# Performance work log

Measured on AMD Instinct MI355X. Metric: run time of the kernel, lower is better.

The kernel has to match this reference:

```python
import jax, jax.numpy as jnp
import numpy as np

G = 16                 # grid side -> 4096 voxels
N_GRID = G ** 3
N_NODES = 4096         # protein nodes
DEG = 256              # node neighbors per grid voxel
HID = 64               # MPNN hidden == ResNet in_channels
NUM_CLASSES = 20
BN = np.float32(1.0 / np.sqrt(1.0 + 1e-5))  # eval-mode BatchNorm3d (mean=0, var=1, gamma=1, beta=0)


def _lin(key, fi, fo):
    return jax.random.normal(key, (fi, fo), jnp.float32) * (fi ** -0.5)


def _cw(key, o, i, k):
    return jax.random.normal(key, (o, i, k, k, k), jnp.float32) * ((i * k ** 3) ** -0.5)


def setup_inputs() -> dict:
    key = jax.random.key(0)
    ks = jax.random.split(key, 32)
    n_edges = N_GRID * DEG
    # every grid voxel receives exactly DEG messages (bincount never zero)
    edge_i = jax.random.randint(ks[0], (n_edges,), 0, N_NODES, dtype=jnp.int32)
    edge_j = jnp.repeat(jnp.arange(N_GRID, dtype=jnp.int32), DEG)
    edge_index = jnp.stack([edge_i, edge_j])  # [2, E]

    node_embedding = jax.random.normal(ks[1], (N_NODES, HID), jnp.float32)
    node_pos = jax.random.uniform(ks[2], (N_NODES, 3), jnp.float32)
    gx = (jnp.arange(G, dtype=jnp.float32) + 0.5) / G
    gd, gh, gw = jnp.meshgrid(gx, gx, gx, indexing='ij')
    grid_pos = jnp.stack([gd, gh, gw], -1).reshape(N_GRID, 3)

    z = lambda n: jnp.zeros((n,), jnp.float32)
    return {
        'node_embedding': node_embedding, 'node_pos': node_pos,
        'grid_pos': grid_pos, 'edge_index': edge_index,
        # MPNN edge / message / update MLPs
        'ew1': _lin(ks[3], 6, HID), 'eb1': z(HID), 'ew2': _lin(ks[4], HID, HID), 'eb2': z(HID),
        'mw1': _lin(ks[5], 2 * HID, HID), 'mb1': z(HID), 'mw2': _lin(ks[6], HID, HID), 'mb2': z(HID),
        'uw1': _lin(ks[7], HID, HID), 'ub1': z(HID), 'uw2': _lin(ks[8], HID, HID), 'ub2': z(HID),
        # ResNet3D: 3 Blocks (conv3 a, conv3 b, conv5 shortcut) with channels 64->64, 64->128, 128->256
        'c1a': _cw(ks[9], 64, 64, 3), 'c1b': _cw(ks[10], 64, 64, 3), 'c1s': _cw(ks[11], 64, 64, 5),
        'c2a': _cw(ks[12], 128, 64, 3), 'c2b': _cw(ks[13], 128, 128, 3), 'c2s': _cw(ks[14], 128, 64, 5),
        'c3a': _cw(ks[15], 256, 128, 3), 'c3b': _cw(ks[16], 256, 256, 3), 'c3s': _cw(ks[17], 256, 128, 5),
        'fcw': _lin(ks[18], 256, NUM_CLASSES), 'fcb': z(NUM_CLASSES),
    }


def _mlp(x, w1, b1, w2, b2):
    return jax.nn.silu(x @ w1 + b1) @ w2 + b2


def _conv(x, w, p):
    return jax.lax.conv_general_dilated(
        x, w, window_strides=(1, 1, 1), padding=[(p, p)] * 3,
        dimension_numbers=('NCDHW', 'OIDHW', 'NCDHW'))


def _block(x, wa, wb, ws):
    out = jax.nn.relu(_conv(x, wa, 1) * BN)
    out = _conv(out, wb, 1) * BN
    sc = _conv(x, ws, 2) * BN
    return jax.nn.relu(out + sc)


def reference(node_embedding, node_pos, grid_pos, edge_index,
              ew1, eb1, ew2, eb2, mw1, mb1, mw2, mb2, uw1, ub1, uw2, ub2,
              c1a, c1b, c1s, c2a, c2b, c2s, c3a, c3b, c3s, fcw, fcb):
    i, j = edge_index[0], edge_index[1]
    # ---- MPNN: gather, edge MLP, message MLP, scatter-mean, update MLP ----
    edge_attr = jnp.concatenate([node_pos[i], grid_pos[j]], axis=-1)        # [E, 6]
    pos_emb = _mlp(edge_attr, ew1, eb1, ew2, eb2)                           # [E, H]
    msg = _mlp(jnp.concatenate([node_embedding[i], pos_emb], -1),
               mw1, mb1, mw2, mb2)                                          # [E, H]
    agg = jax.ops.segment_sum(msg, j, num_segments=N_GRID)                  # [N_GRID, H]
    cnt = jax.ops.segment_sum(jnp.ones((msg.shape[0],), msg.dtype), j,
                              num_segments=N_GRID)
    grid_feat = _mlp(agg / cnt[:, None], uw1, ub1, uw2, ub2)                # [N_GRID, H]
    # ---- ResNet3D over the grid volume ----
    x = grid_feat.T.reshape(1, HID, G, G, G) * BN                           # instance_norm1 (eval BN)
    x = _block(x, c1a, c1b, c1s)
    x = _block(x, c2a, c2b, c2s)
    x = _block(x, c3a, c3b, c3s)
    pooled = jnp.max(x, axis=(2, 3, 4))                                     # max_pool3d(kernel=spatial)
    return pooled @ fcw + fcb                                               # [1, NUM_CLASSES]
```

## Files before the change

### kernel.cpp

```cpp
#include <hip/hip_runtime.h>
#include <math.h>

#define BN_S 0.9999950000374997f

typedef _Float16 half8 __attribute__((ext_vector_type(8)));
typedef float f32x4 __attribute__((ext_vector_type(4)));

__device__ __forceinline__ float silu_f(float x) {
    return __fdividef(x, 1.0f + __expf(-x));
}

__device__ __forceinline__ void gld16(const void* g, void* l) {
    __builtin_amdgcn_global_load_lds(
        (const __attribute__((address_space(1))) void*)g,
        (__attribute__((address_space(3))) void*)l, 16, 0, 0);
}

__global__ __launch_bounds__(64) void prep_w_k(
    const float* __restrict__ ew2, const float* __restrict__ mw1,
    const float* __restrict__ mw2, const float* __restrict__ uw1,
    const float* __restrict__ mb2, const float* __restrict__ ub1,
    float* __restrict__ W_mu, float* __restrict__ b_mu,
    _Float16* __restrict__ wemt_h, _Float16* __restrict__ wemt_l)
{
    const int k = blockIdx.x, c = threadIdx.x;
    float s = 0.f;
    for (int m = 0; m < 64; m++) s = fmaf(ew2[k*64 + m], mw1[(64 + m)*64 + c], s);
    {
        const int q = k >> 5, kg = (k >> 3) & 3, jj = k & 7;
        const int sl = q*256 + c*4 + kg;
        const int p = sl ^ ((sl >> 3) & 7);
        const _Float16 h = (_Float16)s;
        const _Float16 l = (_Float16)(s - (float)h);
        wemt_h[p*8 + jj] = h;
        wemt_l[p*8 + jj] = l;
    }
    float s2 = 0.f;
    for (int m = 0; m < 64; m++) s2 = fmaf(mw2[k*64 + m], uw1[m*64 + c], s2);
    W_mu[k*64 + c] = s2;
    if (k == 0) {
        float s3 = ub1[c];
        for (int m = 0; m < 64; m++) s3 = fmaf(mb2[m], uw1[m*64 + c], s3);
        b_mu[c] = s3;
    }
}

__global__ __launch_bounds__(64) void prep_nodes_k(
    const float* __restrict__ node_embedding, const float* __restrict__ node_pos,
    const float* __restrict__ grid_pos, const float* __restrict__ ew1,
    const float* __restrict__ eb1, const float* __restrict__ mw1,
    const float* __restrict__ mb1, const float* __restrict__ eb2,
    float* __restrict__ a_node, float* __restrict__ g_vox, float* __restrict__ n_node)
{
    const int v = blockIdx.x, c = threadIdx.x;
    const float p0 = node_pos[v*3], p1 = node_pos[v*3 + 1], p2 = node_pos[v*3 + 2];
    a_node[v*64 + c] = fmaf(p0, ew1[c], fmaf(p1, ew1[64 + c], fmaf(p2, ew1[128 + c], eb1[c])));
    const float q0 = grid_pos[v*3], q1 = grid_pos[v*3 + 1], q2 = grid_pos[v*3 + 2];
    g_vox[v*64 + c] = fmaf(q0, ew1[192 + c], fmaf(q1, ew1[256 + c], q2 * ew1[320 + c]));
    float s = mb1[c];
    for (int k = 0; k < 64; k++) s = fmaf(node_embedding[v*64 + k], mw1[k*64 + c], s);
    for (int k = 0; k < 64; k++) s = fmaf(eb2[k], mw1[(64 + k)*64 + c], s);
    n_node[v*64 + c] = s;
}

template<int K3, int NCOG, int NCH>
__global__ __launch_bounds__(256) void wsplit_k(
    const float* __restrict__ w, _Float16* __restrict__ dh, _Float16* __restrict__ dl,
    int CI)
{
    __shared__ float s[32*K3];
    const int co = blockIdx.x, cig = blockIdx.y, t = threadIdx.x;
    const float* src = w + ((size_t)co*CI + cig*32)*K3;
    for (int m = t; m < 32*K3; m += 256) s[m] = src[m];
    __syncthreads();
    const int coG = co >> 6, col = co & 63;
    for (int m = t; m < 32*K3; m += 256) {
        const int tap = m >> 5, cil = m & 31;
        const float x = s[cil*K3 + tap];
        const _Float16 h = (_Float16)x;
        const _Float16 l = (_Float16)(x - (float)h);
        const int b = cil >> 3, jj = cil & 7;
        const int sl = col*4 + b;
        const int p = sl ^ ((sl >> 3) & 7);
        const size_t base = ((size_t)(tap*NCOG + coG)*NCH + cig) * 2048;
        dh[base + p*8 + jj] = h;
        dl[base + p*8 + jj] = l;
    }
}

__global__ __launch_bounds__(256) void edge_kernel(
    const int* __restrict__ edge_i,
    const float* __restrict__ a_node, const float* __restrict__ g_vox,
    const float* __restrict__ n_node,
    const _Float16* __restrict__ wemt_h, const _Float16* __restrict__ wemt_l,
    const float* __restrict__ W_mu, const float* __restrict__ b_mu,
    const float* __restrict__ uw2, const float* __restrict__ ub2,
    _Float16* __restrict__ x0h, _Float16* __restrict__ x0l)
{
    __shared__ __align__(16) _Float16 sAh[4096], sAl[4096];
    __shared__ __align__(16) _Float16 sBh[4096], sBl[4096];
    __shared__ float sV1[64], sV2[64];

    const int j = blockIdx.x, t = threadIdx.x;
    const int lane = t & 63, wv = t >> 6, ln15 = lane & 15, kg = lane >> 4;
    const int ebase = j << 8;

    gld16(wemt_h + t*8, &sAh[t*8]);
    gld16(wemt_h + 2048 + t*8, &sAh[2048 + t*8]);
    gld16(wemt_l + t*8, &sAl[t*8]);
    gld16(wemt_l + 2048 + t*8, &sAl[2048 + t*8]);

    const int r = t >> 2, sub = t & 3;
    float gv[16];
    #pragma unroll
    for (int m = 0; m < 16; m++) gv[m] = g_vox[j*64 + sub*16 + m];

    asm volatile("s_waitcnt vmcnt(0)" ::: "memory");
    __syncthreads();

    float psum[4] = {0.f, 0.f, 0.f, 0.f};

    for (int T = 0; T < 4; T++) {
        {
            const int i = edge_i[ebase + T*64 + r];
            float s1[16];
            #pragma unroll
            for (int m = 0; m < 16; m++)
                s1[m] = silu_f(a_node[i*64 + sub*16 + m] + gv[m]);
            half8 h0, l0, h1, l1;
            #pragma unroll
            for (int m = 0; m < 8; m++) {
                h0[m] = (_Float16)s1[m];
                l0[m] = (_Float16)(s1[m] - (float)h0[m]);
                h1[m] = (_Float16)s1[8 + m];
                l1[m] = (_Float16)(s1[8 + m] - (float)h1[m]);
            }
            const int q = sub >> 1, kg0 = (sub & 1) * 2;
            const int slot0 = (q*4 + kg0)*64 + r;
            *(half8*)&sBh[slot0*8] = h0; *(half8*)&sBl[slot0*8] = l0;
            *(half8*)&sBh[(slot0 + 64)*8] = h1; *(half8*)&sBl[(slot0 + 64)*8] = l1;
        }
        __syncthreads();
        #pragma unroll
        for (int eF = 0; eF < 4; eF++) {
            const int e = eF*16 + ln15;
            const int ie = edge_i[ebase + T*64 + e];
            f32x4 acc;
            {
                const float4 nv = *(const float4*)&n_node[(size_t)ie*64 + wv*16 + kg*4];
                acc[0] = nv.x; acc[1] = nv.y; acc[2] = nv.z; acc[3] = nv.w;
            }
            #pragma unroll
            for (int q = 0; q < 2; q++) {
                const int sa = q*256 + (wv*16 + ln15)*4 + kg;
                const int pa = sa ^ ((sa >> 3) & 7);
                const half8 Ah = *(const half8*)&sAh[pa*8];
                const half8 Al = *(const half8*)&sAl[pa*8];
                const int sb = ((q*4 + kg)*64 + e)*8;
                const half8 Bh = *(const half8*)&sBh[sb];
                const half8 Bl = *(const half8*)&sBl[sb];
                acc = __builtin_amdgcn_mfma_f32_16x16x32_f16(Ah, Bh, acc, 0, 0, 0);
                acc = __builtin_amdgcn_mfma_f32_16x16x32_f16(Ah, Bl, acc, 0, 0, 0);
                acc = __builtin_amdgcn_mfma_f32_16x16x32_f16(Al, Bh, acc, 0, 0, 0);
            }
            #pragma unroll
            for (int rg = 0; rg < 4; rg++) psum[rg] += silu_f(acc[rg]);
        }
        __syncthreads();
    }

    #pragma unroll
    for (int rg = 0; rg < 4; rg++) {
        float v = psum[rg];
        v += __shfl_xor(v, 1, 64); v += __shfl_xor(v, 2, 64);
        v += __shfl_xor(v, 4, 64); v += __shfl_xor(v, 8, 64);
        psum[rg] = v;
    }
    if (ln15 == 0) {
        #pragma unroll
        for (int rg = 0; rg < 4; rg++)
            sV1[wv*16 + kg*4 + rg] = psum[rg] * (1.0f / 256.0f);
    }
    __syncthreads();
    if (t < 64) {
        float h = b_mu[t];
        for (int k = 0; k < 64; k++) h = fmaf(sV1[k], W_mu[k*64 + t], h);
        sV2[t] = silu_f(h);
    }
    __syncthreads();
    if (t < 64) {
        float g = ub2[t];
        for (int k = 0; k < 64; k++) g = fmaf(sV2[k], uw2[k*64 + t], g);
        const float val = g * BN_S;
        const _Float16 hh = (_Float16)val;
        const _Float16 ll = (_Float16)(val - (float)hh);
        const int c = t, zz = j >> 8, v = j & 255;
        const size_t a16 = ((size_t)((c >> 5)*16 + zz)*1024 + ((c >> 3) & 3)*256 + v)*8 + (c & 7);
        x0h[a16] = hh; x0l[a16] = ll;
    }
}

template<int KK, int CI, int NCOG, int CIS>
__global__ __launch_bounds__(256) void conv_mfma_k(
    const _Float16* __restrict__ xh, const _Float16* __restrict__ xl,
    const _Float16* __restrict__ wh, const _Float16* __restrict__ wl,
    float* __restrict__ slab)
{
    constexpr int P = KK/2, K2 = KK*KK, NCH = CI/32, NCHS = NCH/CIS, CO = NCOG*64;
    const int d0 = blockIdx.x, coG = blockIdx.y;
    const int cis = blockIdx.z / KK, kd = blockIdx.z % KK;
    const int t = threadIdx.x;
    const int lane = t & 63, wv = t >> 6;
    const int ln15 = lane & 15, kg = lane >> 4;

    float* sout = slab + ((size_t)blockIdx.z*CO + coG*64)*4096 + d0*256;
    const int z = d0 + kd - P;
    if ((unsigned)z >= 16u) {
        for (int m = t; m < 64*256; m += 256)
            sout[(size_t)(m >> 8)*4096 + (m & 255)] = 0.f;
        return;
    }

    __shared__ __align__(16) _Float16 sXh[8192];
    __shared__ __align__(16) _Float16 sXl[8192];
    __shared__ __align__(16) _Float16 sAh[2][2048];
    __shared__ __align__(16) _Float16 sAl[2][2048];
    __shared__ __align__(16) _Float16 zb[8];
    if (t < 8) zb[t] = (_Float16)0.f;

    auto stage_X = [&](int ch) {
        const size_t b16 = ((size_t)ch*16 + z) * 8192;
        #pragma unroll
        for (int q = 0; q < 4; q++) {
            gld16(xh + b16 + (q*256 + t)*8, &sXh[(q*256 + t)*8]);
            gld16(xl + b16 + (q*256 + t)*8, &sXl[(q*256 + t)*8]);
        }
    };
    auto stage_A = [&](int ab, int ch, int t2) {
        const size_t b16 = ((size_t)((kd*K2 + t2)*NCOG + coG)*NCH + ch) * 2048;
        gld16(wh + b16 + t*8, &sAh[ab][t*8]);
        gld16(wl + b16 + t*8, &sAl[ab][t*8]);
    };

    f32x4 acc[4][4];
    #pragma unroll
    for (int a = 0; a < 4; a++)
        #pragma unroll
        for (int b = 0; b < 4; b++)
            #pragma unroll
            for (int r2 = 0; r2 < 4; r2++) acc[a][b][r2] = 0.f;

    const int ch0 = cis * NCHS;
    stage_A(0, ch0, 0);
    stage_X(ch0);
    asm volatile("s_waitcnt vmcnt(0)" ::: "memory");
    __syncthreads();

    int ap = 0;
    for (int cc = 0; cc < NCHS; cc++) {
        const int ch = ch0 + cc;
        for (int t2 = 0; t2 < K2; t2++) {
            if (t2 + 1 < K2) stage_A(ap ^ 1, ch, t2 + 1);
            else if (cc + 1 < NCHS) stage_A(ap ^ 1, ch + 1, 0);

            const int kh = t2 / KK, kw = t2 % KK;
            half8 Afh[4], Afl[4];
            #pragma unroll
            for (int cf = 0; cf < 4; cf++) {
                const int s = (cf*16 + ln15)*4 + kg;
                const int p = s ^ ((s >> 3) & 7);
                Afh[cf] = *(const half8*)&sAh[ap][p*8];
                Afl[cf] = *(const half8*)&sAl[ap][p*8];
            }
            __builtin_amdgcn_s_setprio(1);
            #pragma unroll
            for (int f = 0; f < 4; f++) {
                const int h_in = wv*4 + f + kh - P;
                if ((unsigned)h_in < 16u) {
                    const int w_in = ln15 + kw - P;
                    const bool ok = (unsigned)w_in < 16u;
                    const int slot = ok ? (kg*256 + h_in*16 + w_in) : 0;
                    const half8 Bh = ok ? *(const half8*)&sXh[slot*8] : *(const half8*)zb;
                    const half8 Bl = ok ? *(const half8*)&sXl[slot*8] : *(const half8*)zb;
                    #pragma unroll
                    for (int cf = 0; cf < 4; cf++) {
                        acc[cf][f] = __builtin_amdgcn_mfma_f32_16x16x32_f16(Afh[cf], Bh, acc[cf][f], 0, 0, 0);
                        acc[cf][f] = __builtin_amdgcn_mfma_f32_16x16x32_f16(Afh[cf], Bl, acc[cf][f], 0, 0, 0);
                        acc[cf][f] = __builtin_amdgcn_mfma_f32_16x16x32_f16(Afl[cf], Bh, acc[cf][f], 0, 0, 0);
                    }
                }
            }
            __builtin_amdgcn_s_setprio(0);
            if (t2 == K2 - 1) {
                __syncthreads();
                if (cc + 1 < NCHS) stage_X(ch + 1);
            }
            asm volatile("s_waitcnt vmcnt(0)" ::: "memory");
            __syncthreads();
            ap ^= 1;
        }
    }

    #pragma unroll
    for (int cf = 0; cf < 4; cf++)
        #pragma unroll
        for (int f = 0; f < 4; f++)
            #pragma unroll
            for (int r2 = 0; r2 < 4; r2++)
                sout[(size_t)(cf*16 + kg*4 + r2)*4096 + wv*64 + f*16 + ln15] = acc[cf][f][r2];
}

template<int S, int RMODE, int OUT>
__global__ __launch_bounds__(256) void reduce_k(
    const float* __restrict__ pbuf, const float* __restrict__ addsrc,
    float* __restrict__ outf, _Float16* __restrict__ oh, _Float16* __restrict__ ol,
    int CO)
{
    const int z = blockIdx.x, c8 = blockIdx.y, v = threadIdx.x;
    float val[8];
    #pragma unroll
    for (int jj = 0; jj < 8; jj++) {
        const int c = c8*8 + jj;
        float a = 0.f;
        #pragma unroll
        for (int s = 0; s < S; s++)
            a += pbuf[((size_t)s*CO + c)*4096 + z*256 + v];
        a *= BN_S;
        if (RMODE == 3) a += addsrc[(size_t)c*4096 + z*256 + v];
        if (RMODE != 2) a = fmaxf(a, 0.f);
        val[jj] = a;
    }
    if (OUT == 0) {
        #pragma unroll
        for (int jj = 0; jj < 8; jj++)
            outf[(size_t)(c8*8 + jj)*4096 + z*256 + v] = val[jj];
    } else if (OUT == 1) {
        half8 hv, lv;
        #pragma unroll
        for (int jj = 0; jj < 8; jj++) {
            hv[jj] = (_Float16)val[jj];
            lv[jj] = (_Float16)(val[jj] - (float)hv[jj]);
        }
        const size_t a16 = ((size_t)((c8 >> 2)*16 + z)*1024 + (c8 & 3)*256 + v)*8;
        *(half8*)&oh[a16] = hv;
        *(half8*)&ol[a16] = lv;
    } else {
        __shared__ float sm[4][8];
        #pragma unroll
        for (int jj = 0; jj < 8; jj++) {
            float m = val[jj];
            m = fmaxf(m, __shfl_xor(m, 1, 64));  m = fmaxf(m, __shfl_xor(m, 2, 64));
            m = fmaxf(m, __shfl_xor(m, 4, 64));  m = fmaxf(m, __shfl_xor(m, 8, 64));
            m = fmaxf(m, __shfl_xor(m, 16, 64)); m = fmaxf(m, __shfl_xor(m, 32, 64));
            if ((v & 63) == 0) sm[v >> 6][jj] = m;
        }
        __syncthreads();
        if (v < 8) {
            const float m = fmaxf(fmaxf(sm[0][v], sm[1][v]), fmaxf(sm[2][v], sm[3][v]));
            outf[z*CO + c8*8 + v] = m;
        }
    }
}

__global__ __launch_bounds__(256) void fc_k(
    const float* __restrict__ pp, const float* __restrict__ fcw,
    const float* __restrict__ fcb, float* __restrict__ out)
{
    __shared__ float sp[256];
    const int t = threadIdx.x;
    float m = pp[t];
    for (int zz = 1; zz < 16; zz++) m = fmaxf(m, pp[zz*256 + t]);
    sp[t] = m;
    __syncthreads();
    if (t < 20) {
        float s = fcb[t];
        for (int c = 0; c < 256; c++) s = fmaf(sp[c], fcw[c*20 + t], s);
        out[t] = s;
    }
}

extern "C" void kernel_launch(void* const* d_in, const int* in_sizes, int n_in,
                              void* d_out, int out_size, void* d_ws, size_t ws_size,
                              hipStream_t stream)
{
    const float* node_embedding = (const float*)d_in[0];
    const float* node_pos       = (const float*)d_in[1];
    const float* grid_pos       = (const float*)d_in[2];
    const int*   edge_index     = (const int*)d_in[3];
    const float* ew1 = (const float*)d_in[4];
    const float* eb1 = (const float*)d_in[5];
    const float* ew2 = (const float*)d_in[6];
    const float* eb2 = (const float*)d_in[7];
    const float* mw1 = (const float*)d_in[8];
    const float* mb1 = (const float*)d_in[9];
    const float* mw2 = (const float*)d_in[10];
    const float* mb2 = (const float*)d_in[11];
    const float* uw1 = (const float*)d_in[12];
    const float* ub1 = (const float*)d_in[13];
    const float* uw2 = (const float*)d_in[14];
    const float* ub2 = (const float*)d_in[15];
    const float* c1a = (const float*)d_in[16];
    const float* c1b = (const float*)d_in[17];
    const float* c1s = (const float*)d_in[18];
    const float* c2a = (const float*)d_in[19];
    const float* c2b = (const float*)d_in[20];
    const float* c2s = (const float*)d_in[21];
    const float* c3a = (const float*)d_in[22];
    const float* c3b = (const float*)d_in[23];
    const float* c3s = (const float*)d_in[24];
    const float* fcw = (const float*)d_in[25];
    const float* fcb = (const float*)d_in[26];
    float* out = (float*)d_out;
    const int* edge_i = edge_index;

    float* ws = (float*)d_ws;
    float* a_node = ws;                ws += 262144;
    float* g_vox  = ws;                ws += 262144;
    float* n_node = ws;                ws += 262144;
    float* W_mu   = ws;                ws += 4096;
    float* b_mu   = ws;                ws += 64;
    _Float16* wemt_h = (_Float16*)ws;  ws += 2048;
    _Float16* wemt_l = (_Float16*)ws;  ws += 2048;
    _Float16* x0h = (_Float16*)ws;     ws += 131072;
    _Float16* x0l = (_Float16*)ws;     ws += 131072;
    _Float16* t2h = (_Float16*)ws;     ws += 262144;
    _Float16* t2l = (_Float16*)ws;     ws += 262144;
    _Float16* x2h = (_Float16*)ws;     ws += 262144;
    _Float16* x2l = (_Float16*)ws;     ws += 262144;
    _Float16* t3h = (_Float16*)ws;     ws += 524288;
    _Float16* t3l = (_Float16*)ws;     ws += 524288;
    float* u2 = ws;                    ws += 524288;
    float* u3 = ws;                    ws += 1048576;
    float* slab = ws;                  ws += 5242880;
    float* poolPart = ws;              ws += 4096;
    _Float16* wh = (_Float16*)ws;      ws += 4585472;
    _Float16* wl = (_Float16*)ws;      ws += 4585472;
    _Float16* t1h = (_Float16*)a_node;
    _Float16* t1l = (_Float16*)(a_node + 131072);
    float* u1 = g_vox;
    _Float16* x1h = (_Float16*)n_node;
    _Float16* x1l = (_Float16*)(n_node + 131072);

    _Float16* w1a_h = wh + 0;       _Float16* w1a_l = wl + 0;
    _Float16* w1b_h = wh + 110592;  _Float16* w1b_l = wl + 110592;
    _Float16* w1s_h = wh + 221184;  _Float16* w1s_l = wl + 221184;
    _Float16* w2a_h = wh + 733184;  _Float16* w2a_l = wl + 733184;
    _Float16* w2b_h = wh + 954368;  _Float16* w2b_l = wl + 954368;
    _Float16* w2s_h = wh + 1396736; _Float16* w2s_l = wl + 1396736;
    _Float16* w3a_h = wh + 2420736; _Float16* w3a_l = wl + 2420736;
    _Float16* w3b_h = wh + 3305472; _Float16* w3b_l = wl + 3305472;
    _Float16* w3s_h = wh + 5074944; _Float16* w3s_l = wl + 5074944;

    hipLaunchKernelGGL((wsplit_k<27,1,2>),  dim3(64,2),  dim3(256), 0, stream, c1a, w1a_h, w1a_l, 64);
    hipLaunchKernelGGL((wsplit_k<27,1,2>),  dim3(64,2),  dim3(256), 0, stream, c1b, w1b_h, w1b_l, 64);
    hipLaunchKernelGGL((wsplit_k<125,1,2>), dim3(64,2),  dim3(256), 0, stream, c1s, w1s_h, w1s_l, 64);
    hipLaunchKernelGGL((wsplit_k<27,2,2>),  dim3(128,2), dim3(256), 0, stream, c2a, w2a_h, w2a_l, 64);
    hipLaunchKernelGGL((wsplit_k<27,2,4>),  dim3(128,4), dim3(256), 0, stream, c2b, w2b_h, w2b_l, 128);
    hipLaunchKernelGGL((wsplit_k<125,2,2>), dim3(128,2), dim3(256), 0, stream, c2s, w2s_h, w2s_l, 64);
    hipLaunchKernelGGL((wsplit_k<27,4,4>),  dim3(256,4), dim3(256), 0, stream, c3a, w3a_h, w3a_l, 128);
    hipLaunchKernelGGL((wsplit_k<27,4,8>),  dim3(256,8), dim3(256), 0, stream, c3b, w3b_h, w3b_l, 256);
    hipLaunchKernelGGL((wsplit_k<125,4,4>), dim3(256,4), dim3(256), 0, stream, c3s, w3s_h, w3s_l, 128);

    hipLaunchKernelGGL(prep_w_k, dim3(64), dim3(64), 0, stream,
                       ew2, mw1, mw2, uw1, mb2, ub1, W_mu, b_mu, wemt_h, wemt_l);
    hipLaunchKernelGGL(prep_nodes_k, dim3(4096), dim3(64), 0, stream,
                       node_embedding, node_pos, grid_pos, ew1, eb1, mw1, mb1, eb2,
                       a_node, g_vox, n_node);
    hipLaunchKernelGGL(edge_kernel, dim3(4096), dim3(256), 0, stream,
                       edge_i, a_node, g_vox, n_node, wemt_h, wemt_l,
                       W_mu, b_mu, uw2, ub2, x0h, x0l);

    hipLaunchKernelGGL((conv_mfma_k<3,64,1,2>), dim3(16,1,6), dim3(256), 0, stream, x0h, x0l, w1a_h, w1a_l, slab);
    hipLaunchKernelGGL((reduce_k<6,1,1>), dim3(16,8), dim3(256), 0, stream, slab, (const float*)nullptr, (float*)nullptr, t1h, t1l, 64);
    hipLaunchKernelGGL((conv_mfma_k<3,64,1,2>), dim3(16,1,6), dim3(256), 0, stream, t1h, t1l, w1b_h, w1b_l, slab);
    hipLaunchKernelGGL((reduce_k<6,2,0>), dim3(16,8), dim3(256), 0, stream, slab, (const float*)nullptr, u1, (_Float16*)nullptr, (_Float16*)nullptr, 64);
    hipLaunchKernelGGL((conv_mfma_k<5,64,1,2>), dim3(16,1,10), dim3(256), 0, stream, x0h, x0l, w1s_h, w1s_l, slab);
    hipLaunchKernelGGL((reduce_k<10,3,1>), dim3(16,8), dim3(256), 0, stream, slab, u1, (float*)nullptr, x1h, x1l, 64);
    hipLaunchKernelGGL((conv_mfma_k<3,64,2,2>), dim3(16,2,6), dim3(256), 0, stream, x1h, x1l, w2a_h, w2a_l, slab);
    hipLaunchKernelGGL((reduce_k<6,1,1>), dim3(16,16), dim3(256), 0, stream, slab, (const float*)nullptr, (float*)nullptr, t2h, t2l, 128);
    hipLaunchKernelGGL((conv_mfma_k<3,128,2,2>), dim3(16,2,6), dim3(256), 0, stream, t2h, t2l, w2b_h, w2b_l, slab);
    hipLaunchKernelGGL((reduce_k<6,2,0>), dim3(16,16), dim3(256), 0, stream, slab, (const float*)nullptr, u2, (_Float16*)nullptr, (_Float16*)nullptr, 128);
    hipLaunchKernelGGL((conv_mfma_k<5,64,2,2>), dim3(16,2,10), dim3(256), 0, stream, x1h, x1l, w2s_h, w2s_l, slab);
    hipLaunchKernelGGL((reduce_k<10,3,1>), dim3(16,16), dim3(256), 0, stream, slab, u2, (float*)nullptr, x2h, x2l, 128);
    hipLaunchKernelGGL((conv_mfma_k<3,128,4,1>), dim3(16,4,3), dim3(256), 0, stream, x2h, x2l, w3a_h, w3a_l, slab);
    hipLaunchKernelGGL((reduce_k<3,1,1>), dim3(16,32), dim3(256), 0, stream, slab, (const float*)nullptr, (float*)nullptr, t3h, t3l, 256);
    hipLaunchKernelGGL((conv_mfma_k<3,256,4,1>), dim3(16,4,3), dim3(256), 0, stream, t3h, t3l, w3b_h, w3b_l, slab);
    hipLaunchKernelGGL((reduce_k<3,2,0>), dim3(16,32), dim3(256), 0, stream, slab, (const float*)nullptr, u3, (_Float16*)nullptr, (_Float16*)nullptr, 256);
    hipLaunchKernelGGL((conv_mfma_k<5,128,4,1>), dim3(16,4,5), dim3(256), 0, stream, x2h, x2l, w3s_h, w3s_l, slab);
    hipLaunchKernelGGL((reduce_k<5,3,2>), dim3(16,32), dim3(256), 0, stream, slab, u3, poolPart, (_Float16*)nullptr, (_Float16*)nullptr, 256);

    hipLaunchKernelGGL(fc_k, dim3(1), dim3(256), 0, stream, poolPart, fcw, fcb, out);

    (void)in_sizes; (void)n_in; (void)out_size; (void)ws_size;
}
```

Baseline: 583.5 us.

## Prefetch conv weights into registers and double-buffer activation tiles in LDS

The implicit-GEMM conv kernel now loads each tap's weight fragments straight from global memory into registers, one tap ahead, instead of staging them through double-buffered LDS. The input activation slab gets two LDS buffers, so the next channel chunk loads while the current one is consumed. This removes the per-tap vmcnt wait and the block barriers, leaving one barrier per channel chunk, so MFMA work overlaps with memory traffic. The cost is more registers and uncoalesced per-lane global weight reads. It also relies on implicit ordering of the async LDS loads before the chunk barrier.

Measured after the change: 529.7 us. 1.1x faster.

```diff
diff --git a/kernel.cpp b/kernel.cpp
--- a/kernel.cpp
+++ b/kernel.cpp
@@ -221,25 +221,33 @@
         return;
     }
 
-    __shared__ __align__(16) _Float16 sXh[8192];
-    __shared__ __align__(16) _Float16 sXl[8192];
-    __shared__ __align__(16) _Float16 sAh[2][2048];
-    __shared__ __align__(16) _Float16 sAl[2][2048];
+    __shared__ __align__(16) _Float16 sXh[2][8192];
+    __shared__ __align__(16) _Float16 sXl[2][8192];
     __shared__ __align__(16) _Float16 zb[8];
     if (t < 8) zb[t] = (_Float16)0.f;
 
-    auto stage_X = [&](int ch) {
+    int aoff[4];
+    #pragma unroll
+    for (int cf = 0; cf < 4; cf++) {
+        const int s = (cf*16 + ln15)*4 + kg;
+        aoff[cf] = (s ^ ((s >> 3) & 7)) * 8;
+    }
+
+    auto stage_X = [&](int xb, int ch) {
         const size_t b16 = ((size_t)ch*16 + z) * 8192;
         #pragma unroll
         for (int q = 0; q < 4; q++) {
-            gld16(xh + b16 + (q*256 + t)*8, &sXh[(q*256 + t)*8]);
-            gld16(xl + b16 + (q*256 + t)*8, &sXl[(q*256 + t)*8]);
+            gld16(xh + b16 + (q*256 + t)*8, &sXh[xb][(q*256 + t)*8]);
+            gld16(xl + b16 + (q*256 + t)*8, &sXl[xb][(q*256 + t)*8]);
         }
     };
-    auto stage_A = [&](int ab, int ch, int t2) {
-        const size_t b16 = ((size_t)((kd*K2 + t2)*NCOG + coG)*NCH + ch) * 2048;
-        gld16(wh + b16 + t*8, &sAh[ab][t*8]);
-        gld16(wl + b16 + t*8, &sAl[ab][t*8]);
+    auto loadA = [&](int ch, int t2, half8* Ah, half8* Al) {
+        const size_t b = ((size_t)((kd*K2 + t2)*NCOG + coG)*NCH + ch) * 2048;
+        #pragma unroll
+        for (int cf = 0; cf < 4; cf++) {
+            Ah[cf] = *(const half8*)&wh[b + aoff[cf]];
+            Al[cf] = *(const half8*)&wl[b + aoff[cf]];
+        }
     };
 
     f32x4 acc[4][4];
@@ -251,27 +259,23 @@
             for (int r2 = 0; r2 < 4; r2++) acc[a][b][r2] = 0.f;
 
     const int ch0 = cis * NCHS;
-    stage_A(0, ch0, 0);
-    stage_X(ch0);
+    half8 nAh[4], nAl[4];
+    stage_X(0, ch0);
+    loadA(ch0, 0, nAh, nAl);
     asm volatile("s_waitcnt vmcnt(0)" ::: "memory");
     __syncthreads();
 
-    int ap = 0;
     for (int cc = 0; cc < NCHS; cc++) {
-        const int ch = ch0 + cc;
+        const int ch = ch0 + cc, xb = cc & 1;
+        if (cc + 1 < NCHS) stage_X(xb ^ 1, ch + 1);
         for (int t2 = 0; t2 < K2; t2++) {
-            if (t2 + 1 < K2) stage_A(ap ^ 1, ch, t2 + 1);
-            else if (cc + 1 < NCHS) stage_A(ap ^ 1, ch + 1, 0);
+            half8 cAh[4], cAl[4];
+            #pragma unroll
+            for (int cf = 0; cf < 4; cf++) { cAh[cf] = nAh[cf]; cAl[cf] = nAl[cf]; }
+            if (t2 + 1 < K2)          loadA(ch, t2 + 1, nAh, nAl);
+            else if (cc + 1 < NCHS)   loadA(ch + 1, 0, nAh, nAl);
 
             const int kh = t2 / KK, kw = t2 % KK;
-            half8 Afh[4], Afl[4];
-            #pragma unroll
-            for (int cf = 0; cf < 4; cf++) {
-                const int s = (cf*16 + ln15)*4 + kg;
-                const int p = s ^ ((s >> 3) & 7);
-                Afh[cf] = *(const half8*)&sAh[ap][p*8];
-                Afl[cf] = *(const half8*)&sAl[ap][p*8];
-            }
             __builtin_amdgcn_s_setprio(1);
             #pragma unroll
             for (int f = 0; f < 4; f++) {
@@ -280,25 +284,19 @@
                     const int w_in = ln15 + kw - P;
                     const bool ok = (unsigned)w_in < 16u;
                     const int slot = ok ? (kg*256 + h_in*16 + w_in) : 0;
-                    const half8 Bh = ok ? *(const half8*)&sXh[slot*8] : *(const half8*)zb;
-                    const half8 Bl = ok ? *(const half8*)&sXl[slot*8] : *(const half8*)zb;
+                    const half8 Bh = ok ? *(const half8*)&sXh[xb][slot*8] : *(const half8*)zb;
+                    const half8 Bl = ok ? *(const half8*)&sXl[xb][slot*8] : *(const half8*)zb;
                     #pragma unroll
                     for (int cf = 0; cf < 4; cf++) {
-                        acc[cf][f] = __builtin_amdgcn_mfma_f32_16x16x32_f16(Afh[cf], Bh, acc[cf][f], 0, 0, 0);
-                        acc[cf][f] = __builtin_amdgcn_mfma_f32_16x16x32_f16(Afh[cf], Bl, acc[cf][f], 0, 0, 0);
-                        acc[cf][f] = __builtin_amdgcn_mfma_f32_16x16x32_f16(Afl[cf], Bh, acc[cf][f], 0, 0, 0);
+                        acc[cf][f] = __builtin_amdgcn_mfma_f32_16x16x32_f16(cAh[cf], Bh, acc[cf][f], 0, 0, 0);
+                        acc[cf][f] = __builtin_amdgcn_mfma_f32_16x16x32_f16(cAh[cf], Bl, acc[cf][f], 0, 0, 0);
+                        acc[cf][f] = __builtin_amdgcn_mfma_f32_16x16x32_f16(cAl[cf], Bh, acc[cf][f], 0, 0, 0);
                     }
                 }
             }
             __builtin_amdgcn_s_setprio(0);
-            if (t2 == K2 - 1) {
-                __syncthreads();
-                if (cc + 1 < NCHS) stage_X(ch + 1);
-            }
-            asm volatile("s_waitcnt vmcnt(0)" ::: "memory");
-            __syncthreads();
-            ap ^= 1;
-        }
+        }
+        __syncthreads();
     }
 
     #pragma unroll
```
